# Optimization experiments

Measured on AMD Instinct MI355X. Metric: run time of the kernel, lower is better.

## Reference

```python
import jax, jax.numpy as jnp
import numpy as np
import math


def _sinusoidal_pe(seq_len, hidden_dim, dtype):
    pos = jnp.arange(seq_len, dtype=jnp.float32)[:, None]              # [S,1]
    div = jnp.exp(jnp.arange(0, hidden_dim, 2, dtype=jnp.float32) * (-math.log(10000.0) / hidden_dim))  # [H/2]
    ang = pos * div                                                    # [S,H/2]
    pe = jnp.stack([jnp.sin(ang), jnp.cos(ang)], axis=-1).reshape(seq_len, hidden_dim)  # interleave sin/cos
    return pe.astype(dtype)


def setup_inputs() -> dict:
    key = jax.random.key(0)
    ks = jax.random.split(key, 12)
    B, S, H = 4, 2048, 1024
    scale = 1.0 / math.sqrt(H)
    inp = {
        "x": jax.random.normal(ks[0], (B, S, H), dtype=jnp.float32),
        "mask": jax.random.randint(ks[1], (B, S, S), 0, 2, dtype=jnp.int32),
        "Wq": jax.random.normal(ks[2], (H, H), dtype=jnp.float32) * scale,
        "bq": jax.random.normal(ks[3], (H,), dtype=jnp.float32) * 0.02,
        "Wk": jax.random.normal(ks[4], (H, H), dtype=jnp.float32) * scale,
        "bk": jax.random.normal(ks[5], (H,), dtype=jnp.float32) * 0.02,
        "Wv": jax.random.normal(ks[6], (H, H), dtype=jnp.float32) * scale,
        "bv": jax.random.normal(ks[7], (H,), dtype=jnp.float32) * 0.02,
        "pos_bias": jax.random.normal(ks[8], (S, S), dtype=jnp.float32),
        "Wo": jax.random.normal(ks[9], (H, H), dtype=jnp.float32) * scale,
        "bo": jax.random.normal(ks[10], (H,), dtype=jnp.float32) * 0.02,
        "gamma": jnp.ones((H,), dtype=jnp.float32),
        "beta": jnp.zeros((H,), dtype=jnp.float32),
    }
    return inp


def reference(x, mask, Wq, bq, Wk, bk, Wv, bv, pos_bias, Wo, bo, gamma, beta):
    B, S, H = x.shape
    scale = math.sqrt(H)
    pe = _sinusoidal_pe(S, H, x.dtype)                  # [S,H]
    xp = x + pe[None, :, :]                             # [B,S,H]
    # torch Linear: y = x @ W.T + b
    q = jnp.einsum('bsh,oh->bso', xp, Wq) + bq
    k = jnp.einsum('bsh,oh->bso', xp, Wk) + bk
    v = jnp.einsum('bsh,oh->bso', xp, Wv) + bv
    scores = jnp.einsum('bqh,bkh->bqk', q, k) / scale   # [B,S,S]
    scores = scores + pos_bias[None, :S, :S]
    scores = jnp.where(mask == 0, jnp.asarray(-1e9, scores.dtype), scores)
    attn = jax.nn.softmax(scores, axis=-1)              # dropout = identity (eval mode)
    context = jnp.einsum('bqk,bkh->bqh', attn, v)
    out = jnp.einsum('bsh,oh->bso', context, Wo) + bo
    # LayerNorm(out + x)
    h = out + x
    mu = jnp.mean(h, axis=-1, keepdims=True)
    var = jnp.var(h, axis=-1, keepdims=True)
    normed = (h - mu) * jax.lax.rsqrt(var + 1e-5) * gamma + beta
    return normed, attn
```

## Files before the change

kernel.cpp:

```cpp
#include <hip/hip_runtime.h>
#include <hip/hip_bf16.h>
#include <math.h>

typedef __hip_bfloat16 bf16;
typedef __bf16 bf16x8 __attribute__((ext_vector_type(8)));
typedef float f32x4 __attribute__((ext_vector_type(4)));

static constexpr int  B_  = 4, S_ = 2048, H_ = 1024;
static constexpr long BSH = (long)B_ * S_ * H_;
static constexpr long SH  = (long)S_ * H_;
static constexpr long SS  = (long)S_ * S_;
static constexpr long HH  = (long)H_ * H_;

#define GLOAD_LDS16(gp, lp)                                                          \
  __builtin_amdgcn_global_load_lds((__attribute__((address_space(1))) void*)(gp),    \
                                   (__attribute__((address_space(3))) void*)(lp),    \
                                   16, 0, 0)

__device__ __forceinline__ float wave_reduce_sum(float v) {
#pragma unroll
  for (int o = 32; o; o >>= 1) v += __shfl_xor(v, o, 64);
  return v;
}
__device__ __forceinline__ float bf16r(float v) {
  return __bfloat162float(__float2bfloat16(v));
}

__global__ void prep_kernel(const float* __restrict__ Wq, const float* __restrict__ Wk,
                            const float* __restrict__ Wv, const float* __restrict__ Wo,
                            bf16* __restrict__ wdst,
                            const float* __restrict__ x, bf16* __restrict__ xpb) {
  const int bx  = blockIdx.x;
  const int tid = threadIdx.x;
  if (bx < 4096) {
    const int w = bx >> 10;
    const float* src = (w == 0) ? Wq : (w == 1) ? Wk : (w == 2) ? Wv : Wo;
    bf16* d = wdst + (long)w * HH;
    const int idx = ((bx & 1023) << 8) + tid;
    const float4 f = ((const float4*)src)[idx];
    d[idx * 4 + 0] = __float2bfloat16(f.x);
    d[idx * 4 + 1] = __float2bfloat16(f.y);
    d[idx * 4 + 2] = __float2bfloat16(f.z);
    d[idx * 4 + 3] = __float2bfloat16(f.w);
  } else {
    const long idx = (((long)(bx - 4096)) << 8) + tid;
    const int  i   = (int)(idx & (H_ / 2 - 1));
    const long bs  = idx >> 9;
    const int  s   = (int)(bs & (S_ - 1));
    const float div = __expf((float)(2 * i) * (-9.210340371976184f / (float)H_));
    const float ang = (float)s * div;
    const float2 xv = ((const float2*)x)[idx];
    xpb[idx * 2 + 0] = __float2bfloat16(xv.x + sinf(ang));
    xpb[idx * 2 + 1] = __float2bfloat16(xv.y + cosf(ang));
  }
}

template <int MODE>
__global__ void gemm_nt(const bf16* __restrict__ A, long sA,
                        const bf16* __restrict__ Bm, long sB,
                        bf16* __restrict__ Cb, float* __restrict__ Cf, long sC,
                        int M, int N, int K,
                        const float* __restrict__ bias0,
                        const float* __restrict__ bias1,
                        const float* __restrict__ bias2,
                        const float* __restrict__ pos_bias,
                        const int* __restrict__ mask,
                        const float* __restrict__ xres,
                        const float* __restrict__ inv_sum) {
  constexpr int BM = 128, BN = 128, BK = 32;
  __shared__ bf16 As[BM * BK];
  __shared__ bf16 Bs[BN * BK];

  const int tid  = threadIdx.x;
  const int lane = tid & 63;
  const int wave = tid >> 6;
  const int wm   = wave & 1;
  const int wn   = wave >> 1;
  const int z    = blockIdx.z;
  const int m0   = blockIdx.x * BM;
  const int n0   = blockIdx.y * BN;

  const bf16* Ab = A  + (long)z * sA;
  const bf16* Bb = Bm + (long)z * sB;

  const int s0 = tid, s1 = tid + 256;
  const bf16* ga0 = Ab + (long)(m0 + (s0 >> 2)) * K + (s0 & 3) * 8;
  const bf16* ga1 = Ab + (long)(m0 + (s1 >> 2)) * K + (s1 & 3) * 8;
  const bf16* gb0 = Bb + (long)(n0 + (s0 >> 2)) * K + (s0 & 3) * 8;
  const bf16* gb1 = Bb + (long)(n0 + (s1 >> 2)) * K + (s1 & 3) * 8;
  bf16* la0 = As + s0 * 8;
  bf16* la1 = As + s1 * 8;
  bf16* lb0 = Bs + s0 * 8;
  bf16* lb1 = Bs + s1 * 8;

  f32x4 acc[4][4] = {};

  const int fr = lane & 15;
  const int fq = (lane >> 4) * 8;

  for (int k0 = 0; k0 < K; k0 += BK) {
    GLOAD_LDS16(ga0 + k0, la0);
    GLOAD_LDS16(ga1 + k0, la1);
    GLOAD_LDS16(gb0 + k0, lb0);
    GLOAD_LDS16(gb1 + k0, lb1);
    __syncthreads();
    bf16x8 af[4], bfv[4];
#pragma unroll
    for (int i = 0; i < 4; ++i) {
      af[i]  = *(const bf16x8*)(As + (wm * 64 + i * 16 + fr) * BK + fq);
      bfv[i] = *(const bf16x8*)(Bs + (wn * 64 + i * 16 + fr) * BK + fq);
    }
#pragma unroll
    for (int i = 0; i < 4; ++i)
#pragma unroll
      for (int j = 0; j < 4; ++j)
        acc[i][j] = __builtin_amdgcn_mfma_f32_16x16x32_bf16(af[i], bfv[j], acc[i][j], 0, 0, 0);
    __syncthreads();
  }

  const float* biasz = (MODE == 0) ? ((z == 0) ? bias0 : (z == 1) ? bias1 : bias2) : bias0;

  const int cc = lane & 15;
  const int cr = (lane >> 4) * 4;
#pragma unroll
  for (int i = 0; i < 4; ++i) {
    const int rowb = m0 + wm * 64 + i * 16 + cr;
#pragma unroll
    for (int j = 0; j < 4; ++j) {
      const int col = n0 + wn * 64 + j * 16 + cc;
#pragma unroll
      for (int r = 0; r < 4; ++r) {
        const int  row  = rowb + r;
        const long loff = (long)row * N + col;
        const long off  = (long)z * sC + loff;
        const float v   = acc[i][j][r];
        if (MODE == 0) {
          Cb[off] = __float2bfloat16(v + biasz[col]);
        } else if (MODE == 1) {
          float sc = v * (1.0f / 32.0f) + pos_bias[loff];
          if (mask[off] == 0) sc = -1e9f;
          Cb[off] = __float2bfloat16(__expf(fminf(sc, 60.0f)));
        } else if (MODE == 2) {
          Cb[off] = __float2bfloat16(v * inv_sum[z * S_ + row]);
        } else {
          Cf[off] = v + biasz[col] + xres[off];
        }
      }
    }
  }
}

__global__ void transpose_kernel(const bf16* __restrict__ v, bf16* __restrict__ vT) {
  __shared__ bf16 tile[64][65];
  const int b     = blockIdx.z;
  const int sBase = blockIdx.x * 64;
  const int hBase = blockIdx.y * 64;
  const bf16* vb  = v  + (long)b * SH;
  bf16*       vTb = vT + (long)b * SH;
  const int tx = threadIdx.x & 63;
  const int ty = threadIdx.x >> 6;
#pragma unroll
  for (int r = ty; r < 64; r += 4)
    tile[r][tx] = vb[(long)(sBase + r) * H_ + hBase + tx];
  __syncthreads();
#pragma unroll
  for (int r = ty; r < 64; r += 4)
    vTb[(long)(hBase + r) * S_ + sBase + tx] = tile[tx][r];
}

__global__ void rownorm_kernel(const bf16* __restrict__ E, float* __restrict__ attn_f,
                               float* __restrict__ inv_sum) {
  const long row = blockIdx.x;
  const int  tid = threadIdx.x;
  const uint4 d = *(const uint4*)(E + row * (long)S_ + tid * 8);
  float ev[8];
  ev[0] = __uint_as_float(d.x << 16); ev[1] = __uint_as_float(d.x & 0xffff0000u);
  ev[2] = __uint_as_float(d.y << 16); ev[3] = __uint_as_float(d.y & 0xffff0000u);
  ev[4] = __uint_as_float(d.z << 16); ev[5] = __uint_as_float(d.z & 0xffff0000u);
  ev[6] = __uint_as_float(d.w << 16); ev[7] = __uint_as_float(d.w & 0xffff0000u);
  float s = 0.f;
#pragma unroll
  for (int i = 0; i < 8; ++i) s += ev[i];
  s = wave_reduce_sum(s);
  __shared__ float red[4];
  if ((tid & 63) == 0) red[tid >> 6] = s;
  __syncthreads();
  const float inv = 1.0f / fmaxf(red[0] + red[1] + red[2] + red[3], 1e-30f);
  if (tid == 0) inv_sum[row] = inv;
  float4 o0, o1;
  o0.x = bf16r(ev[0] * inv); o0.y = bf16r(ev[1] * inv);
  o0.z = bf16r(ev[2] * inv); o0.w = bf16r(ev[3] * inv);
  o1.x = bf16r(ev[4] * inv); o1.y = bf16r(ev[5] * inv);
  o1.z = bf16r(ev[6] * inv); o1.w = bf16r(ev[7] * inv);
  float4* dst = (float4*)(attn_f + row * (long)S_ + tid * 8);
  dst[0] = o0;
  dst[1] = o1;
}

__global__ void ln_kernel(float* __restrict__ h, const float* __restrict__ gamma,
                          const float* __restrict__ beta) {
  const long row = blockIdx.x;
  float* hr = h + row * (long)H_;
  const int tid = threadIdx.x;
  float v[4];
  float s = 0.f;
#pragma unroll
  for (int i = 0; i < 4; ++i) { v[i] = hr[tid + i * 256]; s += v[i]; }
  s = wave_reduce_sum(s);
  __shared__ float redA[4], redB[4];
  if ((tid & 63) == 0) redA[tid >> 6] = s;
  __syncthreads();
  const float mu = (redA[0] + redA[1] + redA[2] + redA[3]) * (1.0f / H_);
  float vs = 0.f;
#pragma unroll
  for (int i = 0; i < 4; ++i) { const float d = v[i] - mu; vs += d * d; }
  vs = wave_reduce_sum(vs);
  if ((tid & 63) == 0) redB[tid >> 6] = vs;
  __syncthreads();
  const float var  = (redB[0] + redB[1] + redB[2] + redB[3]) * (1.0f / H_);
  const float rstd = rsqrtf(var + 1e-5f);
#pragma unroll
  for (int i = 0; i < 4; ++i) {
    const int c = tid + i * 256;
    hr[c] = bf16r((v[i] - mu) * rstd * gamma[c] + beta[c]);
  }
}

extern "C" void kernel_launch(void* const* d_in, const int* in_sizes, int n_in,
                              void* d_out, int out_size, void* d_ws, size_t ws_size,
                              hipStream_t stream) {
  const float* x        = (const float*)d_in[0];
  const int*   mask     = (const int*)d_in[1];
  const float* Wq       = (const float*)d_in[2];
  const float* bq       = (const float*)d_in[3];
  const float* Wk       = (const float*)d_in[4];
  const float* bk       = (const float*)d_in[5];
  const float* Wv       = (const float*)d_in[6];
  const float* bv       = (const float*)d_in[7];
  const float* pos_bias = (const float*)d_in[8];
  const float* Wo       = (const float*)d_in[9];
  const float* bo       = (const float*)d_in[10];
  const float* gamma    = (const float*)d_in[11];
  const float* beta     = (const float*)d_in[12];

  float* normed_f = (float*)d_out;
  float* attn_f   = (float*)((char*)d_out + ((size_t)32 << 20));

  const size_t MiB = (size_t)1 << 20;
  bf16*  xpb     = (bf16*)d_ws;
  bf16*  q_b     = (bf16*)((char*)d_ws +  16 * MiB);
  bf16*  kbuf    = (bf16*)((char*)d_ws +  32 * MiB);
  bf16*  vbuf    = (bf16*)((char*)d_ws +  48 * MiB);
  bf16*  vT      = (bf16*)((char*)d_ws +  64 * MiB);
  bf16*  ctx     = (bf16*)((char*)d_ws +  80 * MiB);
  bf16*  attn_b  = (bf16*)((char*)d_ws +  96 * MiB);
  bf16*  wts     = (bf16*)((char*)d_ws + 128 * MiB);
  float* inv_sum = (float*)((char*)d_ws + 136 * MiB);
  bf16* Wqb = wts, *Wob = wts + 3 * HH;

  const int MQKV = B_ * S_;

  prep_kernel<<<dim3(20480), 256, 0, stream>>>(Wq, Wk, Wv, Wo, wts, x, xpb);

  gemm_nt<0><<<dim3(64, 8, 3), 256, 0, stream>>>(xpb, 0, Wqb, HH, q_b, nullptr, BSH,
                                                 MQKV, H_, H_, bq, bk, bv,
                                                 nullptr, nullptr, nullptr, nullptr);

  transpose_kernel<<<dim3(S_ / 64, H_ / 64, B_), 256, 0, stream>>>(vbuf, vT);

  gemm_nt<1><<<dim3(16, 16, B_), 256, 0, stream>>>(q_b, SH, kbuf, SH,
                                                   attn_b, nullptr, SS,
                                                   S_, S_, H_, nullptr, nullptr, nullptr,
                                                   pos_bias, mask, nullptr, nullptr);

  rownorm_kernel<<<B_ * S_, 256, 0, stream>>>(attn_b, attn_f, inv_sum);

  gemm_nt<2><<<dim3(16, 8, B_), 256, 0, stream>>>(attn_b, SS, vT, SH,
                                                  ctx, nullptr, SH,
                                                  S_, H_, S_, nullptr, nullptr, nullptr,
                                                  nullptr, nullptr, nullptr, inv_sum);

  gemm_nt<3><<<dim3(64, 8, 1), 256, 0, stream>>>(ctx, 0, Wob, 0, nullptr, normed_f, 0,
                                                 MQKV, H_, H_, bo, nullptr, nullptr,
                                                 nullptr, nullptr, x, nullptr);

  ln_kernel<<<B_ * S_, 256, 0, stream>>>(normed_f, gamma, beta);
}
```

Measured before the change: 460.8 us.

## Double-buffer GEMM LDS tiles to overlap global loads with MFMA compute

Splits the shared-memory A/B tiles into two buffers so the next K-slice is loaded directly to LDS while the current slice feeds the MFMAs, with a prologue load and an epilogue compute step. This removes one barrier per iteration and hides global-load latency behind matrix math. It also raises wave priority around the MFMA block with s_setprio. The cost is doubled LDS per block, which may lower occupancy. The compiler's waitcnt for the asynchronous LDS loads at the barrier may also serialize the overlap.

Result: no change. 466.6 us (+1.2%).

```diff
diff --git a/kernel.cpp b/kernel.cpp
--- a/kernel.cpp
+++ b/kernel.cpp
@@ -68,8 +68,8 @@
                         const float* __restrict__ xres,
                         const float* __restrict__ inv_sum) {
   constexpr int BM = 128, BN = 128, BK = 32;
-  __shared__ bf16 As[BM * BK];
-  __shared__ bf16 Bs[BN * BK];
+  __shared__ bf16 As[2][BM * BK];
+  __shared__ bf16 Bs[2][BN * BK];
 
   const int tid  = threadIdx.x;
   const int lane = tid & 63;
@@ -88,34 +88,59 @@
   const bf16* ga1 = Ab + (long)(m0 + (s1 >> 2)) * K + (s1 & 3) * 8;
   const bf16* gb0 = Bb + (long)(n0 + (s0 >> 2)) * K + (s0 & 3) * 8;
   const bf16* gb1 = Bb + (long)(n0 + (s1 >> 2)) * K + (s1 & 3) * 8;
-  bf16* la0 = As + s0 * 8;
-  bf16* la1 = As + s1 * 8;
-  bf16* lb0 = Bs + s0 * 8;
-  bf16* lb1 = Bs + s1 * 8;
+  const int so0 = s0 * 8;
+  const int so1 = s1 * 8;
 
   f32x4 acc[4][4] = {};
 
   const int fr = lane & 15;
   const int fq = (lane >> 4) * 8;
 
-  for (int k0 = 0; k0 < K; k0 += BK) {
-    GLOAD_LDS16(ga0 + k0, la0);
-    GLOAD_LDS16(ga1 + k0, la1);
-    GLOAD_LDS16(gb0 + k0, lb0);
-    GLOAD_LDS16(gb1 + k0, lb1);
-    __syncthreads();
+  GLOAD_LDS16(ga0, &As[0][so0]);
+  GLOAD_LDS16(ga1, &As[0][so1]);
+  GLOAD_LDS16(gb0, &Bs[0][so0]);
+  GLOAD_LDS16(gb1, &Bs[0][so1]);
+  __syncthreads();
+
+  int cur = 0;
+  for (int k0 = BK; k0 < K; k0 += BK) {
+    const int nxt = cur ^ 1;
+    GLOAD_LDS16(ga0 + k0, &As[nxt][so0]);
+    GLOAD_LDS16(ga1 + k0, &As[nxt][so1]);
+    GLOAD_LDS16(gb0 + k0, &Bs[nxt][so0]);
+    GLOAD_LDS16(gb1 + k0, &Bs[nxt][so1]);
+
     bf16x8 af[4], bfv[4];
 #pragma unroll
     for (int i = 0; i < 4; ++i) {
-      af[i]  = *(const bf16x8*)(As + (wm * 64 + i * 16 + fr) * BK + fq);
-      bfv[i] = *(const bf16x8*)(Bs + (wn * 64 + i * 16 + fr) * BK + fq);
+      af[i]  = *(const bf16x8*)(&As[cur][(wm * 64 + i * 16 + fr) * BK + fq]);
+      bfv[i] = *(const bf16x8*)(&Bs[cur][(wn * 64 + i * 16 + fr) * BK + fq]);
     }
+    __builtin_amdgcn_s_setprio(1);
 #pragma unroll
     for (int i = 0; i < 4; ++i)
 #pragma unroll
       for (int j = 0; j < 4; ++j)
         acc[i][j] = __builtin_amdgcn_mfma_f32_16x16x32_bf16(af[i], bfv[j], acc[i][j], 0, 0, 0);
+    __builtin_amdgcn_s_setprio(0);
     __syncthreads();
+    cur ^= 1;
+  }
+
+  {
+    bf16x8 af[4], bfv[4];
+#pragma unroll
+    for (int i = 0; i < 4; ++i) {
+      af[i]  = *(const bf16x8*)(&As[cur][(wm * 64 + i * 16 + fr) * BK + fq]);
+      bfv[i] = *(const bf16x8*)(&Bs[cur][(wn * 64 + i * 16 + fr) * BK + fq]);
+    }
+    __builtin_amdgcn_s_setprio(1);
+#pragma unroll
+    for (int i = 0; i < 4; ++i)
+#pragma unroll
+      for (int j = 0; j < 4; ++j)
+        acc[i][j] = __builtin_amdgcn_mfma_f32_16x16x32_bf16(af[i], bfv[j], acc[i][j], 0, 0, 0);
+    __builtin_amdgcn_s_setprio(0);
   }
 
   const float* biasz = (MODE == 0) ? ((z == 0) ? bias0 : (z == 1) ? bias1 : bias2) : bias0;
```

## Rewrite GEMM with 256-row tiles, 4-stage async LDS pipeline and swizzle

Applied to the files above, without the earlier changes.

The tiled GEMM now uses 512 threads and 256xBN tiles, with BN=256 for the QK^T scores GEMM. Global-to-LDS loads run through a 4-buffer pipeline with explicit vmcnt waits and a single barrier per k-step. LDS rows are XOR-swizzled to reduce bank conflicts, and setprio is raised around the MFMA bursts. The aim is to hide global load latency and cut barrier overhead, at the cost of much larger LDS use (up to 128KB), which limits occupancy to one block per CU, and fewer blocks in the grid.

Result: slower. 482.3 us (+4.7%).

```diff
diff --git a/kernel.cpp b/kernel.cpp
--- a/kernel.cpp
+++ b/kernel.cpp
@@ -16,6 +16,16 @@
   __builtin_amdgcn_global_load_lds((__attribute__((address_space(1))) void*)(gp),    \
                                    (__attribute__((address_space(3))) void*)(lp),    \
                                    16, 0, 0)
+
+#define BARRIER() do { __builtin_amdgcn_s_barrier(); asm volatile("" ::: "memory"); } while (0)
+
+template <int N> __device__ __forceinline__ void waitcnt_vm() {
+  if constexpr (N == 0)      asm volatile("s_waitcnt vmcnt(0)" ::: "memory");
+  else if constexpr (N == 3) asm volatile("s_waitcnt vmcnt(3)" ::: "memory");
+  else if constexpr (N == 4) asm volatile("s_waitcnt vmcnt(4)" ::: "memory");
+  else if constexpr (N == 6) asm volatile("s_waitcnt vmcnt(6)" ::: "memory");
+  else if constexpr (N == 8) asm volatile("s_waitcnt vmcnt(8)" ::: "memory");
+}
 
 __device__ __forceinline__ float wave_reduce_sum(float v) {
 #pragma unroll
@@ -55,85 +65,115 @@
   }
 }
 
-template <int MODE>
-__global__ void gemm_nt(const bf16* __restrict__ A, long sA,
-                        const bf16* __restrict__ Bm, long sB,
-                        bf16* __restrict__ Cb, float* __restrict__ Cf, long sC,
-                        int M, int N, int K,
-                        const float* __restrict__ bias0,
-                        const float* __restrict__ bias1,
-                        const float* __restrict__ bias2,
-                        const float* __restrict__ pos_bias,
-                        const int* __restrict__ mask,
-                        const float* __restrict__ xres,
-                        const float* __restrict__ inv_sum) {
-  constexpr int BM = 128, BN = 128, BK = 32;
-  __shared__ bf16 As[BM * BK];
-  __shared__ bf16 Bs[BN * BK];
-
-  const int tid  = threadIdx.x;
-  const int lane = tid & 63;
-  const int wave = tid >> 6;
-  const int wm   = wave & 1;
-  const int wn   = wave >> 1;
+template <int MODE, int BN>
+__global__ __launch_bounds__(512, 2)
+void gemm_nt(const bf16* __restrict__ A, long strideA,
+             const bf16* __restrict__ Bm, long strideB,
+             bf16* __restrict__ Cb, float* __restrict__ Cf, long sC,
+             int M, int N, int K,
+             const float* __restrict__ bias0,
+             const float* __restrict__ bias1,
+             const float* __restrict__ bias2,
+             const float* __restrict__ pos_bias,
+             const int* __restrict__ mask,
+             const float* __restrict__ xres,
+             const float* __restrict__ inv_sum) {
+  constexpr int BM = 256, BK = 32;
+  constexpr int FN    = BN / 64;
+  constexpr int LPT_B = BN * BK * 2 / 8192;
+  constexpr int LPT   = 2 + LPT_B;
+
+  __shared__ bf16 sA[4][BM * BK];
+  __shared__ bf16 sB[4][BN * BK];
+
+  const int t    = threadIdx.x;
+  const int lane = t & 63;
+  const int wave = t >> 6;
+  const int wm   = wave >> 2;
+  const int wn   = wave & 3;
   const int z    = blockIdx.z;
   const int m0   = blockIdx.x * BM;
   const int n0   = blockIdx.y * BN;
 
-  const bf16* Ab = A  + (long)z * sA;
-  const bf16* Bb = Bm + (long)z * sB;
-
-  const int s0 = tid, s1 = tid + 256;
-  const bf16* ga0 = Ab + (long)(m0 + (s0 >> 2)) * K + (s0 & 3) * 8;
-  const bf16* ga1 = Ab + (long)(m0 + (s1 >> 2)) * K + (s1 & 3) * 8;
-  const bf16* gb0 = Bb + (long)(n0 + (s0 >> 2)) * K + (s0 & 3) * 8;
-  const bf16* gb1 = Bb + (long)(n0 + (s1 >> 2)) * K + (s1 & 3) * 8;
-  bf16* la0 = As + s0 * 8;
-  bf16* la1 = As + s1 * 8;
-  bf16* lb0 = Bs + s0 * 8;
-  bf16* lb1 = Bs + s1 * 8;
-
-  f32x4 acc[4][4] = {};
-
-  const int fr = lane & 15;
-  const int fq = (lane >> 4) * 8;
-
-  for (int k0 = 0; k0 < K; k0 += BK) {
-    GLOAD_LDS16(ga0 + k0, la0);
-    GLOAD_LDS16(ga1 + k0, la1);
-    GLOAD_LDS16(gb0 + k0, lb0);
-    GLOAD_LDS16(gb1 + k0, lb1);
-    __syncthreads();
-    bf16x8 af[4], bfv[4];
-#pragma unroll
-    for (int i = 0; i < 4; ++i) {
-      af[i]  = *(const bf16x8*)(As + (wm * 64 + i * 16 + fr) * BK + fq);
-      bfv[i] = *(const bf16x8*)(Bs + (wn * 64 + i * 16 + fr) * BK + fq);
+  const bf16* Ab = A  + (long)z * strideA;
+  const bf16* Bb = Bm + (long)z * strideB;
+
+  const int rS  = t >> 2, pS = t & 3;
+  const int swS = (rS >> 1) & 3;
+  const bf16* gA0 = Ab + (long)(m0 + rS)       * K + (pS ^ swS) * 8;
+  const bf16* gA1 = Ab + (long)(m0 + rS + 128) * K + (pS ^ swS) * 8;
+  const bf16* gB0 = Bb + (long)(n0 + rS)       * K + (pS ^ swS) * 8;
+  const bf16* gB1 = Bb + (long)(n0 + rS + 128) * K + (pS ^ swS) * 8;
+
+  auto stage = [&](int tileIdx) {
+    const int buf = tileIdx & 3;
+    const int k0  = tileIdx * BK;
+    GLOAD_LDS16(gA0 + k0, &sA[buf][t * 8]);
+    GLOAD_LDS16(gA1 + k0, &sA[buf][(t + 512) * 8]);
+    GLOAD_LDS16(gB0 + k0, &sB[buf][t * 8]);
+    if constexpr (BN == 256) GLOAD_LDS16(gB1 + k0, &sB[buf][(t + 512) * 8]);
+  };
+
+  const int fr  = lane & 15;
+  const int cqs = ((lane >> 4) << 4) ^ (((fr >> 1) & 3) << 4);
+
+  f32x4 acc[8][FN] = {};
+
+  auto tile_compute = [&](int buf) {
+    const char* bA = (const char*)&sA[buf][0];
+    const char* bB = (const char*)&sB[buf][0];
+    bf16x8 bfv[FN];
+#pragma unroll
+    for (int j = 0; j < FN; ++j)
+      bfv[j] = *(const bf16x8*)(bB + (wn * (BN / 4) + j * 16 + fr) * 64 + cqs);
+#pragma unroll
+    for (int qm = 0; qm < 2; ++qm) {
+      bf16x8 af[4];
+#pragma unroll
+      for (int i = 0; i < 4; ++i)
+        af[i] = *(const bf16x8*)(bA + (wm * 128 + qm * 64 + i * 16 + fr) * 64 + cqs);
+      __builtin_amdgcn_s_setprio(1);
+#pragma unroll
+      for (int i = 0; i < 4; ++i)
+#pragma unroll
+        for (int j = 0; j < FN; ++j)
+          acc[qm * 4 + i][j] =
+              __builtin_amdgcn_mfma_f32_16x16x32_bf16(af[i], bfv[j], acc[qm * 4 + i][j], 0, 0, 0);
+      __builtin_amdgcn_s_setprio(0);
     }
-#pragma unroll
-    for (int i = 0; i < 4; ++i)
-#pragma unroll
-      for (int j = 0; j < 4; ++j)
-        acc[i][j] = __builtin_amdgcn_mfma_f32_16x16x32_bf16(af[i], bfv[j], acc[i][j], 0, 0, 0);
-    __syncthreads();
+  };
+
+  const int nkt = K / BK;
+  stage(0); stage(1); stage(2);
+  for (int kt = 0; kt < nkt - 2; ++kt) {
+    waitcnt_vm<2 * LPT>();
+    BARRIER();
+    if (kt + 3 < nkt) stage(kt + 3);
+    tile_compute(kt & 3);
   }
+  waitcnt_vm<LPT>();
+  BARRIER();
+  tile_compute((nkt - 2) & 3);
+  waitcnt_vm<0>();
+  BARRIER();
+  tile_compute((nkt - 1) & 3);
 
   const float* biasz = (MODE == 0) ? ((z == 0) ? bias0 : (z == 1) ? bias1 : bias2) : bias0;
 
   const int cc = lane & 15;
   const int cr = (lane >> 4) * 4;
 #pragma unroll
-  for (int i = 0; i < 4; ++i) {
-    const int rowb = m0 + wm * 64 + i * 16 + cr;
-#pragma unroll
-    for (int j = 0; j < 4; ++j) {
-      const int col = n0 + wn * 64 + j * 16 + cc;
+  for (int mi = 0; mi < 8; ++mi) {
+    const int rowb = m0 + wm * 128 + mi * 16 + cr;
+#pragma unroll
+    for (int j = 0; j < FN; ++j) {
+      const int col = n0 + wn * (BN / 4) + j * 16 + cc;
 #pragma unroll
       for (int r = 0; r < 4; ++r) {
         const int  row  = rowb + r;
         const long loff = (long)row * N + col;
         const long off  = (long)z * sC + loff;
-        const float v   = acc[i][j][r];
+        const float v   = acc[mi][j][r];
         if (MODE == 0) {
           Cb[off] = __float2bfloat16(v + biasz[col]);
         } else if (MODE == 1) {
@@ -262,27 +302,27 @@
 
   prep_kernel<<<dim3(20480), 256, 0, stream>>>(Wq, Wk, Wv, Wo, wts, x, xpb);
 
-  gemm_nt<0><<<dim3(64, 8, 3), 256, 0, stream>>>(xpb, 0, Wqb, HH, q_b, nullptr, BSH,
-                                                 MQKV, H_, H_, bq, bk, bv,
-                                                 nullptr, nullptr, nullptr, nullptr);
+  gemm_nt<0, 128><<<dim3(32, 8, 3), 512, 0, stream>>>(xpb, 0, Wqb, HH, q_b, nullptr, BSH,
+                                                      MQKV, H_, H_, bq, bk, bv,
+                                                      nullptr, nullptr, nullptr, nullptr);
 
   transpose_kernel<<<dim3(S_ / 64, H_ / 64, B_), 256, 0, stream>>>(vbuf, vT);
 
-  gemm_nt<1><<<dim3(16, 16, B_), 256, 0, stream>>>(q_b, SH, kbuf, SH,
-                                                   attn_b, nullptr, SS,
-                                                   S_, S_, H_, nullptr, nullptr, nullptr,
-                                                   pos_bias, mask, nullptr, nullptr);
+  gemm_nt<1, 256><<<dim3(8, 8, 4), 512, 0, stream>>>(q_b, SH, kbuf, SH,
+                                                     attn_b, nullptr, SS,
+                                                     S_, S_, H_, nullptr, nullptr, nullptr,
+                                                     pos_bias, mask, nullptr, nullptr);
 
   rownorm_kernel<<<B_ * S_, 256, 0, stream>>>(attn_b, attn_f, inv_sum);
 
-  gemm_nt<2><<<dim3(16, 8, B_), 256, 0, stream>>>(attn_b, SS, vT, SH,
-                                                  ctx, nullptr, SH,
-                                                  S_, H_, S_, nullptr, nullptr, nullptr,
-                                                  nullptr, nullptr, nullptr, inv_sum);
-
-  gemm_nt<3><<<dim3(64, 8, 1), 256, 0, stream>>>(ctx, 0, Wob, 0, nullptr, normed_f, 0,
-                                                 MQKV, H_, H_, bo, nullptr, nullptr,
-                                                 nullptr, nullptr, x, nullptr);
+  gemm_nt<2, 128><<<dim3(8, 8, 4), 512, 0, stream>>>(attn_b, SS, vT, SH,
+                                                     ctx, nullptr, SH,
+                                                     S_, H_, S_, nullptr, nullptr, nullptr,
+                                                     nullptr, nullptr, nullptr, inv_sum);
+
+  gemm_nt<3, 128><<<dim3(32, 8, 1), 512, 0, stream>>>(ctx, 0, Wob, 0, nullptr, normed_f, 0,
+                                                      MQKV, H_, H_, bo, nullptr, nullptr,
+                                                      nullptr, nullptr, x, nullptr);
 
   ln_kernel<<<B_ * S_, 256, 0, stream>>>(normed_f, gamma, beta);
 }
```

## Double GEMM K-tile with XOR-swizzled LDS and bit-pack attention mask

Applied to the files above, without the earlier changes.

Raises the GEMM K-tile from 32 to 64 and XOR-swizzles the LDS layout, which halves the number of barrier pairs per tile and avoids LDS bank conflicts on the fragment reads. The int32 mask is packed into bitwords in the prep kernel, so the score epilogue reads one word per 32 columns instead of one int per element. The positional-encoding sin/cos calls now use the fast __sinf/__cosf intrinsics. The costs are a larger LDS footprint, which may reduce occupancy, an extra pass that reads the full mask once, and lower accuracy from the fast trig.

After: 433.2 us. -6.0%, faster.

```diff
diff --git a/kernel.cpp b/kernel.cpp
--- a/kernel.cpp
+++ b/kernel.cpp
@@ -29,7 +29,8 @@
 __global__ void prep_kernel(const float* __restrict__ Wq, const float* __restrict__ Wk,
                             const float* __restrict__ Wv, const float* __restrict__ Wo,
                             bf16* __restrict__ wdst,
-                            const float* __restrict__ x, bf16* __restrict__ xpb) {
+                            const float* __restrict__ x, bf16* __restrict__ xpb,
+                            const int* __restrict__ mask, unsigned* __restrict__ mask_bits) {
   const int bx  = blockIdx.x;
   const int tid = threadIdx.x;
   if (bx < 4096) {
@@ -42,7 +43,7 @@
     d[idx * 4 + 1] = __float2bfloat16(f.y);
     d[idx * 4 + 2] = __float2bfloat16(f.z);
     d[idx * 4 + 3] = __float2bfloat16(f.w);
-  } else {
+  } else if (bx < 20480) {
     const long idx = (((long)(bx - 4096)) << 8) + tid;
     const int  i   = (int)(idx & (H_ / 2 - 1));
     const long bs  = idx >> 9;
@@ -50,8 +51,21 @@
     const float div = __expf((float)(2 * i) * (-9.210340371976184f / (float)H_));
     const float ang = (float)s * div;
     const float2 xv = ((const float2*)x)[idx];
-    xpb[idx * 2 + 0] = __float2bfloat16(xv.x + sinf(ang));
-    xpb[idx * 2 + 1] = __float2bfloat16(xv.y + cosf(ang));
+    xpb[idx * 2 + 0] = __float2bfloat16(xv.x + __sinf(ang));
+    xpb[idx * 2 + 1] = __float2bfloat16(xv.y + __cosf(ang));
+  } else {
+    const long uidx = (((long)(bx - 20480)) << 8) + tid;
+    const int4* mp  = (const int4*)mask + uidx * 8;
+    unsigned bits = 0;
+#pragma unroll
+    for (int q = 0; q < 8; ++q) {
+      const int4 v = mp[q];
+      bits |= (v.x ? 1u : 0u) << (q * 4 + 0);
+      bits |= (v.y ? 1u : 0u) << (q * 4 + 1);
+      bits |= (v.z ? 1u : 0u) << (q * 4 + 2);
+      bits |= (v.w ? 1u : 0u) << (q * 4 + 3);
+    }
+    mask_bits[uidx] = bits;
   }
 }
 
@@ -64,10 +78,10 @@
                         const float* __restrict__ bias1,
                         const float* __restrict__ bias2,
                         const float* __restrict__ pos_bias,
-                        const int* __restrict__ mask,
+                        const unsigned* __restrict__ mask_bits,
                         const float* __restrict__ xres,
                         const float* __restrict__ inv_sum) {
-  constexpr int BM = 128, BN = 128, BK = 32;
+  constexpr int BM = 128, BN = 128, BK = 64;
   __shared__ bf16 As[BM * BK];
   __shared__ bf16 Bs[BN * BK];
 
@@ -83,38 +97,41 @@
   const bf16* Ab = A  + (long)z * sA;
   const bf16* Bb = Bm + (long)z * sB;
 
-  const int s0 = tid, s1 = tid + 256;
-  const bf16* ga0 = Ab + (long)(m0 + (s0 >> 2)) * K + (s0 & 3) * 8;
-  const bf16* ga1 = Ab + (long)(m0 + (s1 >> 2)) * K + (s1 & 3) * 8;
-  const bf16* gb0 = Bb + (long)(n0 + (s0 >> 2)) * K + (s0 & 3) * 8;
-  const bf16* gb1 = Bb + (long)(n0 + (s1 >> 2)) * K + (s1 & 3) * 8;
-  bf16* la0 = As + s0 * 8;
-  bf16* la1 = As + s1 * 8;
-  bf16* lb0 = Bs + s0 * 8;
-  bf16* lb1 = Bs + s1 * 8;
+  const int rw = tid >> 3;
+  const int cp = (tid & 7) ^ (rw & 7);
+  const bf16* ga = Ab + (long)(m0 + rw) * K + cp * 8;
+  const bf16* gb = Bb + (long)(n0 + rw) * K + cp * 8;
+  bf16* la = As + tid * 8;
+  bf16* lb = Bs + tid * 8;
 
   f32x4 acc[4][4] = {};
 
-  const int fr = lane & 15;
-  const int fq = (lane >> 4) * 8;
+  const int fr     = lane & 15;
+  const int k0slot = lane >> 4;
+  const int sw     = fr & 7;
 
   for (int k0 = 0; k0 < K; k0 += BK) {
-    GLOAD_LDS16(ga0 + k0, la0);
-    GLOAD_LDS16(ga1 + k0, la1);
-    GLOAD_LDS16(gb0 + k0, lb0);
-    GLOAD_LDS16(gb1 + k0, lb1);
+#pragma unroll
+    for (int q = 0; q < 4; ++q) {
+      GLOAD_LDS16(ga + (long)(32 * q) * K + k0, la + q * 2048);
+      GLOAD_LDS16(gb + (long)(32 * q) * K + k0, lb + q * 2048);
+    }
     __syncthreads();
-    bf16x8 af[4], bfv[4];
-#pragma unroll
-    for (int i = 0; i < 4; ++i) {
-      af[i]  = *(const bf16x8*)(As + (wm * 64 + i * 16 + fr) * BK + fq);
-      bfv[i] = *(const bf16x8*)(Bs + (wn * 64 + i * 16 + fr) * BK + fq);
+#pragma unroll
+    for (int ks = 0; ks < 2; ++ks) {
+      const int co = ((k0slot + 4 * ks) ^ sw) << 4;
+      bf16x8 af[4], bfv[4];
+#pragma unroll
+      for (int i = 0; i < 4; ++i) {
+        af[i]  = *(const bf16x8*)((const char*)As + (wm * 64 + i * 16 + fr) * 128 + co);
+        bfv[i] = *(const bf16x8*)((const char*)Bs + (wn * 64 + i * 16 + fr) * 128 + co);
+      }
+#pragma unroll
+      for (int i = 0; i < 4; ++i)
+#pragma unroll
+        for (int j = 0; j < 4; ++j)
+          acc[i][j] = __builtin_amdgcn_mfma_f32_16x16x32_bf16(af[i], bfv[j], acc[i][j], 0, 0, 0);
     }
-#pragma unroll
-    for (int i = 0; i < 4; ++i)
-#pragma unroll
-      for (int j = 0; j < 4; ++j)
-        acc[i][j] = __builtin_amdgcn_mfma_f32_16x16x32_bf16(af[i], bfv[j], acc[i][j], 0, 0, 0);
     __syncthreads();
   }
 
@@ -137,8 +154,9 @@
         if (MODE == 0) {
           Cb[off] = __float2bfloat16(v + biasz[col]);
         } else if (MODE == 1) {
+          const unsigned mw = mask_bits[off >> 5];
           float sc = v * (1.0f / 32.0f) + pos_bias[loff];
-          if (mask[off] == 0) sc = -1e9f;
+          if (((mw >> (col & 31)) & 1u) == 0u) sc = -1e9f;
           Cb[off] = __float2bfloat16(__expf(fminf(sc, 60.0f)));
         } else if (MODE == 2) {
           Cb[off] = __float2bfloat16(v * inv_sum[z * S_ + row]);
@@ -247,20 +265,22 @@
   float* attn_f   = (float*)((char*)d_out + ((size_t)32 << 20));
 
   const size_t MiB = (size_t)1 << 20;
-  bf16*  xpb     = (bf16*)d_ws;
-  bf16*  q_b     = (bf16*)((char*)d_ws +  16 * MiB);
-  bf16*  kbuf    = (bf16*)((char*)d_ws +  32 * MiB);
-  bf16*  vbuf    = (bf16*)((char*)d_ws +  48 * MiB);
-  bf16*  vT      = (bf16*)((char*)d_ws +  64 * MiB);
-  bf16*  ctx     = (bf16*)((char*)d_ws +  80 * MiB);
-  bf16*  attn_b  = (bf16*)((char*)d_ws +  96 * MiB);
-  bf16*  wts     = (bf16*)((char*)d_ws + 128 * MiB);
-  float* inv_sum = (float*)((char*)d_ws + 136 * MiB);
+  bf16*     xpb       = (bf16*)d_ws;
+  bf16*     q_b       = (bf16*)((char*)d_ws +  16 * MiB);
+  bf16*     kbuf      = (bf16*)((char*)d_ws +  32 * MiB);
+  bf16*     vbuf      = (bf16*)((char*)d_ws +  48 * MiB);
+  bf16*     vT        = (bf16*)((char*)d_ws +  64 * MiB);
+  bf16*     ctx       = (bf16*)((char*)d_ws +  80 * MiB);
+  bf16*     attn_b    = (bf16*)((char*)d_ws +  96 * MiB);
+  bf16*     wts       = (bf16*)((char*)d_ws + 128 * MiB);
+  float*    inv_sum   = (float*)((char*)d_ws + 136 * MiB);
+  unsigned* mask_bits = (unsigned*)((char*)d_ws + 137 * MiB);
   bf16* Wqb = wts, *Wob = wts + 3 * HH;
 
   const int MQKV = B_ * S_;
 
-  prep_kernel<<<dim3(20480), 256, 0, stream>>>(Wq, Wk, Wv, Wo, wts, x, xpb);
+  prep_kernel<<<dim3(22528), 256, 0, stream>>>(Wq, Wk, Wv, Wo, wts, x, xpb,
+                                               mask, mask_bits);
 
   gemm_nt<0><<<dim3(64, 8, 3), 256, 0, stream>>>(xpb, 0, Wqb, HH, q_b, nullptr, BSH,
                                                  MQKV, H_, H_, bq, bk, bv,
@@ -271,7 +291,7 @@
   gemm_nt<1><<<dim3(16, 16, B_), 256, 0, stream>>>(q_b, SH, kbuf, SH,
                                                    attn_b, nullptr, SS,
                                                    S_, S_, H_, nullptr, nullptr, nullptr,
-                                                   pos_bias, mask, nullptr, nullptr);
+                                                   pos_bias, mask_bits, nullptr, nullptr);
 
   rownorm_kernel<<<B_ * S_, 256, 0, stream>>>(attn_b, attn_f, inv_sum);
 
```
